# Performance work log

Measured on AMD Instinct MI355X. Metric: run time of the kernel, lower is better.

The kernel has to match this reference:

```python
import jax, jax.numpy as jnp
import numpy as np

D = 512      # feature_bins
DK = 64      # d_k = d_v
H = 8        # n_heads
EPS = 1e-5


def setup_inputs() -> dict:
    key = jax.random.key(0)
    ks = jax.random.split(key, 12)
    B, S = 4, 2048
    s = 1.0 / np.sqrt(D)
    inp = {
        "Q": jax.random.normal(ks[0], (B, S, D), jnp.float32),
        "K": jax.random.normal(ks[1], (B, S, D), jnp.float32),
        "V": jax.random.normal(ks[2], (B, S, D), jnp.float32),
        # nn.Linear params: weight [out, in], bias [out]
        "Wq": jax.random.normal(ks[3], (H * DK, D), jnp.float32) * s,
        "bq": jnp.zeros((H * DK,), jnp.float32),
        "Wk": jax.random.normal(ks[4], (H * DK, D), jnp.float32) * s,
        "bk": jnp.zeros((H * DK,), jnp.float32),
        "Wv": jax.random.normal(ks[5], (H * DK, D), jnp.float32) * s,
        "bv": jnp.zeros((H * DK,), jnp.float32),
        "Wo": jax.random.normal(ks[6], (D, H * DK), jnp.float32) * s,
        "bo": jnp.zeros((D,), jnp.float32),
        "gamma": jnp.ones((D,), jnp.float32),
        "beta": jnp.zeros((D,), jnp.float32),
    }
    return inp


def _layernorm(x, gamma, beta):
    mu = jnp.mean(x, axis=-1, keepdims=True)
    var = jnp.mean(jnp.square(x - mu), axis=-1, keepdims=True)
    return (x - mu) * jax.lax.rsqrt(var + EPS) * gamma + beta


def reference(Q, K, V, Wq, bq, Wk, bk, Wv, bv, Wo, bo, gamma, beta):
    B, S, _ = Q.shape
    residual = Q
    # projections -> [B, H, S, DK]
    q = (Q @ Wq.T + bq).reshape(B, S, H, DK).transpose(0, 2, 1, 3)
    k = (K @ Wk.T + bk).reshape(B, S, H, DK).transpose(0, 2, 1, 3)
    v = (V @ Wv.T + bv).reshape(B, S, H, DK).transpose(0, 2, 1, 3)
    # NOTE: original code has NO 1/sqrt(d_k) scaling
    scores = jnp.einsum("bhqd,bhkd->bhqk", q, k)
    attn = jax.nn.softmax(scores, axis=-1)
    context = jnp.einsum("bhqk,bhkd->bhqd", attn, v)
    context = context.transpose(0, 2, 1, 3).reshape(B, S, H * DK)
    output = context @ Wo.T + bo
    out = _layernorm(output + residual, gamma, beta)
    return (out, attn)
```

## Files before the change

### kernel.cpp

```cpp
#include <hip/hip_runtime.h>

#define NB 4
#define NS 2048
#define ND 512
#define NH 8
#define NDK 64
#define LN_EPS 1e-5f
#define SCLAMP 80.0f

typedef __attribute__((ext_vector_type(8))) short short8;
typedef __attribute__((ext_vector_type(4))) short s16x4;
typedef __attribute__((ext_vector_type(4))) float f32x4;

__device__ inline short f2bf(float x) {
    unsigned u = __builtin_bit_cast(unsigned, x);
    unsigned r = (u + 0x7FFFu + ((u >> 16) & 1u)) >> 16;
    return (short)r;
}
__device__ inline float bf2f(short h) {
    unsigned u = ((unsigned)(unsigned short)h) << 16;
    return __builtin_bit_cast(float, u);
}
__device__ inline unsigned splitT(float x) {
    unsigned u = __builtin_bit_cast(unsigned, x);
    unsigned h = u >> 16;
    float r = x - bf2f((short)h);
    unsigned l = __builtin_bit_cast(unsigned, r) >> 16;
    return (h & 0xFFFFu) | (l << 16);
}

__device__ inline int swzS(int row, int b8) {
    return row * 64 + (((b8) * 8) ^ ((row & 7) << 3));
}
__device__ inline int swz4(int row, int g4) {
    return row * 64 + ((((g4 >> 1)) * 8) ^ ((row & 7) << 3)) + (g4 & 1) * 4;
}

template<int MODE>
__global__ __launch_bounds__(256) void k_projm(
    const float* __restrict__ X, const float* __restrict__ W,
    const float* __restrict__ bias,
    short* __restrict__ outh, short* __restrict__ outl)
{
    __shared__ short WsH[8192], WsL[8192];
    const int tid = threadIdx.x;
    const int w = tid >> 6, lane = tid & 63;
    const int lr = lane & 15, lg = lane >> 4;
    const int row0 = blockIdx.y * 64;
    const int col0 = blockIdx.x * 128;
    const int xrow = row0 + w * 16 + lr;

    f32x4 acc[8] = {};

    float4 wb[8], ab[4];
#pragma unroll
    for (int i = 0; i < 8; ++i) {
        int idx = tid + 256 * i, wrow = idx >> 4, g4 = idx & 15;
        wb[i] = *(const float4*)&W[(size_t)(col0 + wrow) * ND + g4 * 4];
    }
#pragma unroll
    for (int ks = 0; ks < 2; ++ks) {
        ab[2*ks+0] = *(const float4*)&X[(size_t)xrow * ND + ks * 32 + lg * 8];
        ab[2*ks+1] = *(const float4*)&X[(size_t)xrow * ND + ks * 32 + lg * 8 + 4];
    }

    for (int kc = 0; kc < 8; ++kc) {
        __syncthreads();
#pragma unroll
        for (int i = 0; i < 8; ++i) {
            int idx = tid + 256 * i, wrow = idx >> 4, g4 = idx & 15;
            s16x4 hv, lv;
            unsigned p0 = splitT(wb[i].x), p1 = splitT(wb[i].y);
            unsigned p2 = splitT(wb[i].z), p3 = splitT(wb[i].w);
            hv[0] = (short)p0; lv[0] = (short)(p0 >> 16);
            hv[1] = (short)p1; lv[1] = (short)(p1 >> 16);
            hv[2] = (short)p2; lv[2] = (short)(p2 >> 16);
            hv[3] = (short)p3; lv[3] = (short)(p3 >> 16);
            int off = swz4(wrow, g4);
            *(s16x4*)&WsH[off] = hv;
            *(s16x4*)&WsL[off] = lv;
        }
        __syncthreads();

        short8 ah[2], al[2];
#pragma unroll
        for (int ks = 0; ks < 2; ++ks) {
#pragma unroll
            for (int j = 0; j < 4; ++j) {
                unsigned p = splitT(ab[2*ks][j]);
                ah[ks][j] = (short)p; al[ks][j] = (short)(p >> 16);
            }
#pragma unroll
            for (int j = 0; j < 4; ++j) {
                unsigned p = splitT(ab[2*ks+1][j]);
                ah[ks][4+j] = (short)p; al[ks][4+j] = (short)(p >> 16);
            }
        }

        if (kc < 7) {
            const int kn = (kc + 1) * 64;
#pragma unroll
            for (int i = 0; i < 8; ++i) {
                int idx = tid + 256 * i, wrow = idx >> 4, g4 = idx & 15;
                wb[i] = *(const float4*)&W[(size_t)(col0 + wrow) * ND + kn + g4 * 4];
            }
#pragma unroll
            for (int ks = 0; ks < 2; ++ks) {
                ab[2*ks+0] = *(const float4*)&X[(size_t)xrow * ND + kn + ks * 32 + lg * 8];
                ab[2*ks+1] = *(const float4*)&X[(size_t)xrow * ND + kn + ks * 32 + lg * 8 + 4];
            }
        }

#pragma unroll
        for (int cs = 0; cs < 8; ++cs)
#pragma unroll
            for (int ks = 0; ks < 2; ++ks) {
                short8 fh = *(const short8*)&WsH[swzS(cs * 16 + lr, ks * 4 + lg)];
                short8 fl = *(const short8*)&WsL[swzS(cs * 16 + lr, ks * 4 + lg)];
                acc[cs] = __builtin_amdgcn_mfma_f32_16x16x32_bf16(ah[ks], fh, acc[cs], 0, 0, 0);
                acc[cs] = __builtin_amdgcn_mfma_f32_16x16x32_bf16(ah[ks], fl, acc[cs], 0, 0, 0);
                acc[cs] = __builtin_amdgcn_mfma_f32_16x16x32_bf16(al[ks], fh, acc[cs], 0, 0, 0);
            }
    }

#pragma unroll
    for (int cs = 0; cs < 8; ++cs) {
        int c = col0 + cs * 16 + lr;
        int h_ = c >> 6, dk = c & (NDK - 1);
        float bv = bias[c];
#pragma unroll
        for (int r = 0; r < 4; ++r) {
            int gr = row0 + w * 16 + lg * 4 + r;
            int b_ = gr >> 11, s_ = gr & (NS - 1);
            float x = acc[cs][r] + bv;
            if (MODE == 0) {
                size_t idx = (((size_t)b_ * NH + h_) * NS + s_) * NDK + dk;
                short hb = f2bf(x);
                outh[idx] = hb;
                outl[idx] = f2bf(x - bf2f(hb));
            } else {
                size_t idx = (((size_t)b_ * NH + h_) * NDK + dk) * NS + s_;
                outh[idx] = f2bf(x);
            }
        }
    }
}

__device__ inline void att_decode(int wg, int& bh, int& rt) {
    rt = (wg >> 3) & 31;
    bh = (wg & 7) + ((wg >> 8) << 3);
}

__global__ __launch_bounds__(256) void k_pvl(
    const short* __restrict__ qh, const short* __restrict__ ql,
    const short* __restrict__ kh, const short* __restrict__ kl,
    const short* __restrict__ vtb,
    float* __restrict__ iLrow, short* __restrict__ ctxb)
{
    __shared__ short KsH[4096], KsL[4096], Vs[4096];
    __shared__ short plbf[4][16][72];
    const int tid = threadIdx.x;
    const int w = tid >> 6, lane = tid & 63;
    const int lr = lane & 15, lg = lane >> 4;
    int bh, rt;
    att_decode(blockIdx.x, bh, rt);
    const int row0 = rt * 64 + w * 16;
    const size_t base = (size_t)bh * NS * NDK;
    const short* vb = vtb + (size_t)bh * NDK * NS;
    const int srow0 = tid >> 3, sb8 = tid & 7;
    const int srow1 = srow0 + 32;

    short8 ah[2], al[2];
#pragma unroll
    for (int ks = 0; ks < 2; ++ks) {
        size_t idx = base + (size_t)(row0 + lr) * NDK + ks * 32 + lg * 8;
        ah[ks] = *(const short8*)&qh[idx];
        al[ks] = *(const short8*)&ql[idx];
    }

    float lsum[4] = {0.f, 0.f, 0.f, 0.f};
    f32x4 vacc[4] = {};

    short8 nh0, nh1, nl0, nl1, nv0, nv1;
    {
        nh0 = *(const short8*)&kh[base + (size_t)(srow0) * NDK + sb8 * 8];
        nh1 = *(const short8*)&kh[base + (size_t)(srow1) * NDK + sb8 * 8];
        nl0 = *(const short8*)&kl[base + (size_t)(srow0) * NDK + sb8 * 8];
        nl1 = *(const short8*)&kl[base + (size_t)(srow1) * NDK + sb8 * 8];
        nv0 = *(const short8*)&vb[(size_t)srow0 * NS + sb8 * 8];
        nv1 = *(const short8*)&vb[(size_t)srow1 * NS + sb8 * 8];
    }

    for (int c = 0; c < 32; ++c) {
        short8 ch0 = nh0, ch1 = nh1, cl0 = nl0, cl1 = nl1, cv0 = nv0, cv1 = nv1;
        __syncthreads();
        *(short8*)&KsH[swzS(srow0, sb8)] = ch0;
        *(short8*)&KsH[swzS(srow1, sb8)] = ch1;
        *(short8*)&KsL[swzS(srow0, sb8)] = cl0;
        *(short8*)&KsL[swzS(srow1, sb8)] = cl1;
        *(short8*)&Vs[swzS(srow0, sb8)] = cv0;
        *(short8*)&Vs[swzS(srow1, sb8)] = cv1;
        __syncthreads();

        if (c < 31) {
            const int coln = (c + 1) * 64;
            nh0 = *(const short8*)&kh[base + (size_t)(coln + srow0) * NDK + sb8 * 8];
            nh1 = *(const short8*)&kh[base + (size_t)(coln + srow1) * NDK + sb8 * 8];
            nl0 = *(const short8*)&kl[base + (size_t)(coln + srow0) * NDK + sb8 * 8];
            nl1 = *(const short8*)&kl[base + (size_t)(coln + srow1) * NDK + sb8 * 8];
            nv0 = *(const short8*)&vb[(size_t)srow0 * NS + coln + sb8 * 8];
            nv1 = *(const short8*)&vb[(size_t)srow1 * NS + coln + sb8 * 8];
        }

        f32x4 sa[4] = {};
#pragma unroll
        for (int cs = 0; cs < 4; ++cs)
#pragma unroll
            for (int ks = 0; ks < 2; ++ks) {
                short8 fh = *(const short8*)&KsH[swzS(cs * 16 + lr, ks * 4 + lg)];
                short8 fl = *(const short8*)&KsL[swzS(cs * 16 + lr, ks * 4 + lg)];
                sa[cs] = __builtin_amdgcn_mfma_f32_16x16x32_bf16(ah[ks], fh, sa[cs], 0, 0, 0);
                sa[cs] = __builtin_amdgcn_mfma_f32_16x16x32_bf16(ah[ks], fl, sa[cs], 0, 0, 0);
                sa[cs] = __builtin_amdgcn_mfma_f32_16x16x32_bf16(al[ks], fh, sa[cs], 0, 0, 0);
            }

#pragma unroll
        for (int cs = 0; cs < 4; ++cs)
#pragma unroll
            for (int r = 0; r < 4; ++r) {
                float e = __expf(fminf(sa[cs][r], SCLAMP));
                lsum[r] += e;
                plbf[w][lg * 4 + r][cs * 16 + lr] = f2bf(e);
            }
#pragma unroll
        for (int k2 = 0; k2 < 2; ++k2) {
            short8 pa = *(const short8*)&plbf[w][lr][k2 * 32 + lg * 8];
#pragma unroll
            for (int d = 0; d < 4; ++d) {
                short8 vf = *(const short8*)&Vs[swzS(d * 16 + lr, k2 * 4 + lg)];
                vacc[d] = __builtin_amdgcn_mfma_f32_16x16x32_bf16(pa, vf, vacc[d], 0, 0, 0);
            }
        }
    }

#pragma unroll
    for (int r = 0; r < 4; ++r)
#pragma unroll
        for (int off = 1; off < 16; off <<= 1)
            lsum[r] += __shfl_xor(lsum[r], off);

    float iL[4];
#pragma unroll
    for (int r = 0; r < 4; ++r) iL[r] = 1.0f / lsum[r];
    if (lr == 0) {
#pragma unroll
        for (int r = 0; r < 4; ++r)
            iLrow[(size_t)bh * NS + row0 + lg * 4 + r] = iL[r];
    }
    const int b_ = bh >> 3, h_ = bh & 7;
#pragma unroll
    for (int d = 0; d < 4; ++d)
#pragma unroll
        for (int r = 0; r < 4; ++r) {
            int row = row0 + lg * 4 + r;
            ctxb[((size_t)b_ * NS + row) * ND + h_ * NDK + d * 16 + lr] =
                f2bf(vacc[d][r] * iL[r]);
        }
}

__global__ __launch_bounds__(256) void k_attn_write(
    const short* __restrict__ qh, const short* __restrict__ ql,
    const short* __restrict__ kh, const short* __restrict__ kl,
    const float* __restrict__ iLrow, float* __restrict__ attn)
{
    __shared__ short KsH[4096], KsL[4096];
    const int tid = threadIdx.x;
    const int w = tid >> 6, lane = tid & 63;
    const int lr = lane & 15, lg = lane >> 4;
    int bh, rt;
    att_decode(blockIdx.x, bh, rt);
    const int row0 = rt * 64 + w * 16;
    const size_t base = (size_t)bh * NS * NDK;
    float* ab = attn + (size_t)bh * NS * NS;
    const int srow0 = tid >> 3, sb8 = tid & 7;
    const int srow1 = srow0 + 32;

    short8 ah[2], al[2];
#pragma unroll
    for (int ks = 0; ks < 2; ++ks) {
        size_t idx = base + (size_t)(row0 + lr) * NDK + ks * 32 + lg * 8;
        ah[ks] = *(const short8*)&qh[idx];
        al[ks] = *(const short8*)&ql[idx];
    }
    float iLr[4];
#pragma unroll
    for (int r = 0; r < 4; ++r)
        iLr[r] = iLrow[(size_t)bh * NS + row0 + lg * 4 + r];

    short8 nh0, nh1, nl0, nl1;
    {
        nh0 = *(const short8*)&kh[base + (size_t)(srow0) * NDK + sb8 * 8];
        nh1 = *(const short8*)&kh[base + (size_t)(srow1) * NDK + sb8 * 8];
        nl0 = *(const short8*)&kl[base + (size_t)(srow0) * NDK + sb8 * 8];
        nl1 = *(const short8*)&kl[base + (size_t)(srow1) * NDK + sb8 * 8];
    }

    for (int c = 0; c < 32; ++c) {
        short8 ch0 = nh0, ch1 = nh1, cl0 = nl0, cl1 = nl1;
        __syncthreads();
        *(short8*)&KsH[swzS(srow0, sb8)] = ch0;
        *(short8*)&KsH[swzS(srow1, sb8)] = ch1;
        *(short8*)&KsL[swzS(srow0, sb8)] = cl0;
        *(short8*)&KsL[swzS(srow1, sb8)] = cl1;
        __syncthreads();

        if (c < 31) {
            const int coln = (c + 1) * 64;
            nh0 = *(const short8*)&kh[base + (size_t)(coln + srow0) * NDK + sb8 * 8];
            nh1 = *(const short8*)&kh[base + (size_t)(coln + srow1) * NDK + sb8 * 8];
            nl0 = *(const short8*)&kl[base + (size_t)(coln + srow0) * NDK + sb8 * 8];
            nl1 = *(const short8*)&kl[base + (size_t)(coln + srow1) * NDK + sb8 * 8];
        }

        const int col0 = c * 64;
        f32x4 sa[4] = {};
#pragma unroll
        for (int cs = 0; cs < 4; ++cs)
#pragma unroll
            for (int ks = 0; ks < 2; ++ks) {
                short8 fh = *(const short8*)&KsH[swzS(cs * 16 + lr, ks * 4 + lg)];
                short8 fl = *(const short8*)&KsL[swzS(cs * 16 + lr, ks * 4 + lg)];
                sa[cs] = __builtin_amdgcn_mfma_f32_16x16x32_bf16(ah[ks], fh, sa[cs], 0, 0, 0);
                sa[cs] = __builtin_amdgcn_mfma_f32_16x16x32_bf16(ah[ks], fl, sa[cs], 0, 0, 0);
                sa[cs] = __builtin_amdgcn_mfma_f32_16x16x32_bf16(al[ks], fh, sa[cs], 0, 0, 0);
            }

#pragma unroll
        for (int cs = 0; cs < 4; ++cs)
#pragma unroll
            for (int r = 0; r < 4; ++r) {
                float p = __expf(fminf(sa[cs][r], SCLAMP)) * iLr[r];
                ab[(size_t)(row0 + lg * 4 + r) * NS + col0 + cs * 16 + lr] = p;
            }
    }
}

__global__ __launch_bounds__(256) void k_outproj_m(
    const short* __restrict__ Xc, const float* __restrict__ W,
    const float* __restrict__ bias, const float* __restrict__ Qin,
    float* __restrict__ out)
{
    __shared__ short WsH[8192], WsL[8192];
    const int tid = threadIdx.x;
    const int w = tid >> 6, lane = tid & 63;
    const int lr = lane & 15, lg = lane >> 4;
    const int row0 = blockIdx.y * 64;
    const int col0 = blockIdx.x * 128;
    const int xrow = row0 + w * 16 + lr;

    f32x4 acc[8] = {};

    float4 wb[8];
    short8 abn[2];
#pragma unroll
    for (int i = 0; i < 8; ++i) {
        int idx = tid + 256 * i, wrow = idx >> 4, g4 = idx & 15;
        wb[i] = *(const float4*)&W[(size_t)(col0 + wrow) * ND + g4 * 4];
    }
#pragma unroll
    for (int ks = 0; ks < 2; ++ks)
        abn[ks] = *(const short8*)&Xc[(size_t)xrow * ND + ks * 32 + lg * 8];

    for (int kc = 0; kc < 8; ++kc) {
        __syncthreads();
#pragma unroll
        for (int i = 0; i < 8; ++i) {
            int idx = tid + 256 * i, wrow = idx >> 4, g4 = idx & 15;
            s16x4 hv, lv;
            unsigned p0 = splitT(wb[i].x), p1 = splitT(wb[i].y);
            unsigned p2 = splitT(wb[i].z), p3 = splitT(wb[i].w);
            hv[0] = (short)p0; lv[0] = (short)(p0 >> 16);
            hv[1] = (short)p1; lv[1] = (short)(p1 >> 16);
            hv[2] = (short)p2; lv[2] = (short)(p2 >> 16);
            hv[3] = (short)p3; lv[3] = (short)(p3 >> 16);
            int off = swz4(wrow, g4);
            *(s16x4*)&WsH[off] = hv;
            *(s16x4*)&WsL[off] = lv;
        }
        __syncthreads();

        short8 ah[2] = { abn[0], abn[1] };

        if (kc < 7) {
            const int kn = (kc + 1) * 64;
#pragma unroll
            for (int i = 0; i < 8; ++i) {
                int idx = tid + 256 * i, wrow = idx >> 4, g4 = idx & 15;
                wb[i] = *(const float4*)&W[(size_t)(col0 + wrow) * ND + kn + g4 * 4];
            }
#pragma unroll
            for (int ks = 0; ks < 2; ++ks)
                abn[ks] = *(const short8*)&Xc[(size_t)xrow * ND + kn + ks * 32 + lg * 8];
        }

#pragma unroll
        for (int cs = 0; cs < 8; ++cs)
#pragma unroll
            for (int ks = 0; ks < 2; ++ks) {
                short8 fh = *(const short8*)&WsH[swzS(cs * 16 + lr, ks * 4 + lg)];
                short8 fl = *(const short8*)&WsL[swzS(cs * 16 + lr, ks * 4 + lg)];
                acc[cs] = __builtin_amdgcn_mfma_f32_16x16x32_bf16(ah[ks], fh, acc[cs], 0, 0, 0);
                acc[cs] = __builtin_amdgcn_mfma_f32_16x16x32_bf16(ah[ks], fl, acc[cs], 0, 0, 0);
            }
    }

#pragma unroll
    for (int cs = 0; cs < 8; ++cs) {
        int c = col0 + cs * 16 + lr;
        float bv = bias[c];
#pragma unroll
        for (int r = 0; r < 4; ++r) {
            int gr = row0 + w * 16 + lg * 4 + r;
            float res = Qin[(size_t)gr * ND + c];
            out[(size_t)gr * ND + c] = acc[cs][r] + bv + res;
        }
    }
}

__global__ __launch_bounds__(256) void k_ln(
    float* __restrict__ out, const float* __restrict__ gamma,
    const float* __restrict__ beta)
{
    const int tid = threadIdx.x;
    float* p = out + (size_t)blockIdx.x * ND;
    float2 v = *(const float2*)&p[tid * 2];

    float s = v.x + v.y;
#pragma unroll
    for (int off = 32; off > 0; off >>= 1) s += __shfl_xor(s, off);
    __shared__ float red1[4];
    __shared__ float red2[4];
    if ((tid & 63) == 0) red1[tid >> 6] = s;
    __syncthreads();
    const float mu = (red1[0] + red1[1] + red1[2] + red1[3]) * (1.0f / ND);

    float dx = v.x - mu, dy = v.y - mu;
    float q = dx * dx + dy * dy;
#pragma unroll
    for (int off = 32; off > 0; off >>= 1) q += __shfl_xor(q, off);
    if ((tid & 63) == 0) red2[tid >> 6] = q;
    __syncthreads();
    const float var = (red2[0] + red2[1] + red2[2] + red2[3]) * (1.0f / ND);
    const float inv = rsqrtf(var + LN_EPS);

    float2 g = *(const float2*)&gamma[tid * 2];
    float2 be = *(const float2*)&beta[tid * 2];
    float2 o = { dx * inv * g.x + be.x, dy * inv * g.y + be.y };
    *(float2*)&p[tid * 2] = o;
}

extern "C" void kernel_launch(void* const* d_in, const int* in_sizes, int n_in,
                              void* d_out, int out_size, void* d_ws, size_t ws_size,
                              hipStream_t stream)
{
    const float* Q    = (const float*)d_in[0];
    const float* K    = (const float*)d_in[1];
    const float* V    = (const float*)d_in[2];
    const float* Wq   = (const float*)d_in[3];
    const float* bq   = (const float*)d_in[4];
    const float* Wk   = (const float*)d_in[5];
    const float* bk   = (const float*)d_in[6];
    const float* Wv   = (const float*)d_in[7];
    const float* bv   = (const float*)d_in[8];
    const float* Wo   = (const float*)d_in[9];
    const float* bo   = (const float*)d_in[10];
    const float* gam  = (const float*)d_in[11];
    const float* bet  = (const float*)d_in[12];

    float* out  = (float*)d_out;
    float* attn = out + (size_t)NB * NS * ND;

    const size_t QKV = (size_t)NB * NH * NS * NDK;
    short* qh   = (short*)d_ws;
    short* ql   = qh + QKV;
    short* kh   = ql + QKV;
    short* kl   = kh + QKV;
    short* vtb  = kl + QKV;
    short* ctxb = vtb + QKV;
    float* iLrow = (float*)(ctxb + QKV);

    dim3 blk(256);

    dim3 gP(ND / 128, (NB * NS) / 64);
    k_projm<0><<<gP, blk, 0, stream>>>(Q, Wq, bq, qh, ql);
    k_projm<0><<<gP, blk, 0, stream>>>(K, Wk, bk, kh, kl);
    k_projm<1><<<gP, blk, 0, stream>>>(V, Wv, bv, vtb, (short*)nullptr);

    dim3 gAtt((NS / 64) * NB * NH);
    k_pvl<<<gAtt, blk, 0, stream>>>(qh, ql, kh, kl, vtb, iLrow, ctxb);
    k_attn_write<<<gAtt, blk, 0, stream>>>(qh, ql, kh, kl, iLrow, attn);

    dim3 gO(ND / 128, (NB * NS) / 64);
    k_outproj_m<<<gO, blk, 0, stream>>>(ctxb, Wo, bo, Q, out);

    k_ln<<<dim3(NB * NS), blk, 0, stream>>>(out, gam, bet);
}
```

Before: 352.2 us.

## Process two 64-row query subtiles per workgroup in attention kernels

Each workgroup in both attention kernels now covers 128 query rows instead of 64. Every wave handles two 16-row subtiles, so the K and V tiles staged in shared memory are reused twice and the grid shrinks by half. This is meant to cut global and LDS traffic for K/V staging per query row. The cost is more registers for Q fragments and accumulators, plus only 512 workgroups, which may lower occupancy or leave part of the 256 CUs idle.

```diff
diff --git a/kernel.cpp b/kernel.cpp
--- a/kernel.cpp
+++ b/kernel.cpp
@@ -146,9 +146,9 @@
     }
 }
 
-__device__ inline void att_decode(int wg, int& bh, int& rt) {
-    rt = (wg >> 3) & 31;
-    bh = (wg & 7) + ((wg >> 8) << 3);
+__device__ inline void att_decode2(int wg, int& bh, int& rt) {
+    rt = (wg >> 3) & 15;
+    bh = (wg & 7) + ((wg >> 7) << 3);
 }
 
 __global__ __launch_bounds__(256) void k_pvl(
@@ -158,28 +158,30 @@
     float* __restrict__ iLrow, short* __restrict__ ctxb)
 {
     __shared__ short KsH[4096], KsL[4096], Vs[4096];
-    __shared__ short plbf[4][16][72];
+    __shared__ short plbf[4][32][72];
     const int tid = threadIdx.x;
     const int w = tid >> 6, lane = tid & 63;
     const int lr = lane & 15, lg = lane >> 4;
     int bh, rt;
-    att_decode(blockIdx.x, bh, rt);
-    const int row0 = rt * 64 + w * 16;
+    att_decode2(blockIdx.x, bh, rt);
+    const int row0 = rt * 128 + w * 16;
     const size_t base = (size_t)bh * NS * NDK;
     const short* vb = vtb + (size_t)bh * NDK * NS;
     const int srow0 = tid >> 3, sb8 = tid & 7;
     const int srow1 = srow0 + 32;
 
-    short8 ah[2], al[2];
-#pragma unroll
-    for (int ks = 0; ks < 2; ++ks) {
-        size_t idx = base + (size_t)(row0 + lr) * NDK + ks * 32 + lg * 8;
-        ah[ks] = *(const short8*)&qh[idx];
-        al[ks] = *(const short8*)&ql[idx];
-    }
-
-    float lsum[4] = {0.f, 0.f, 0.f, 0.f};
-    f32x4 vacc[4] = {};
+    short8 ah[2][2], al[2][2];
+#pragma unroll
+    for (int st = 0; st < 2; ++st)
+#pragma unroll
+        for (int ks = 0; ks < 2; ++ks) {
+            size_t idx = base + (size_t)(row0 + st * 64 + lr) * NDK + ks * 32 + lg * 8;
+            ah[st][ks] = *(const short8*)&qh[idx];
+            al[st][ks] = *(const short8*)&ql[idx];
+        }
+
+    float lsum[2][4] = {};
+    f32x4 vacc[2][4] = {};
 
     short8 nh0, nh1, nl0, nl1, nv0, nv1;
     {
@@ -212,60 +214,76 @@
             nv1 = *(const short8*)&vb[(size_t)srow1 * NS + coln + sb8 * 8];
         }
 
-        f32x4 sa[4] = {};
+        f32x4 sa[2][4] = {};
 #pragma unroll
         for (int cs = 0; cs < 4; ++cs)
 #pragma unroll
             for (int ks = 0; ks < 2; ++ks) {
                 short8 fh = *(const short8*)&KsH[swzS(cs * 16 + lr, ks * 4 + lg)];
                 short8 fl = *(const short8*)&KsL[swzS(cs * 16 + lr, ks * 4 + lg)];
-                sa[cs] = __builtin_amdgcn_mfma_f32_16x16x32_bf16(ah[ks], fh, sa[cs], 0, 0, 0);
-                sa[cs] = __builtin_amdgcn_mfma_f32_16x16x32_bf16(ah[ks], fl, sa[cs], 0, 0, 0);
-                sa[cs] = __builtin_amdgcn_mfma_f32_16x16x32_bf16(al[ks], fh, sa[cs], 0, 0, 0);
-            }
-
-#pragma unroll
-        for (int cs = 0; cs < 4; ++cs)
-#pragma unroll
-            for (int r = 0; r < 4; ++r) {
-                float e = __expf(fminf(sa[cs][r], SCLAMP));
-                lsum[r] += e;
-                plbf[w][lg * 4 + r][cs * 16 + lr] = f2bf(e);
-            }
+#pragma unroll
+                for (int st = 0; st < 2; ++st) {
+                    sa[st][cs] = __builtin_amdgcn_mfma_f32_16x16x32_bf16(ah[st][ks], fh, sa[st][cs], 0, 0, 0);
+                    sa[st][cs] = __builtin_amdgcn_mfma_f32_16x16x32_bf16(ah[st][ks], fl, sa[st][cs], 0, 0, 0);
+                    sa[st][cs] = __builtin_amdgcn_mfma_f32_16x16x32_bf16(al[st][ks], fh, sa[st][cs], 0, 0, 0);
+                }
+            }
+
+#pragma unroll
+        for (int st = 0; st < 2; ++st)
+#pragma unroll
+            for (int cs = 0; cs < 4; ++cs)
+#pragma unroll
+                for (int r = 0; r < 4; ++r) {
+                    float e = __expf(fminf(sa[st][cs][r], SCLAMP));
+                    lsum[st][r] += e;
+                    plbf[w][st * 16 + lg * 4 + r][cs * 16 + lr] = f2bf(e);
+                }
+
 #pragma unroll
         for (int k2 = 0; k2 < 2; ++k2) {
-            short8 pa = *(const short8*)&plbf[w][lr][k2 * 32 + lg * 8];
+            short8 pa0 = *(const short8*)&plbf[w][lr][k2 * 32 + lg * 8];
+            short8 pa1 = *(const short8*)&plbf[w][16 + lr][k2 * 32 + lg * 8];
 #pragma unroll
             for (int d = 0; d < 4; ++d) {
                 short8 vf = *(const short8*)&Vs[swzS(d * 16 + lr, k2 * 4 + lg)];
-                vacc[d] = __builtin_amdgcn_mfma_f32_16x16x32_bf16(pa, vf, vacc[d], 0, 0, 0);
-            }
-        }
-    }
-
-#pragma unroll
-    for (int r = 0; r < 4; ++r)
-#pragma unroll
-        for (int off = 1; off < 16; off <<= 1)
-            lsum[r] += __shfl_xor(lsum[r], off);
-
-    float iL[4];
-#pragma unroll
-    for (int r = 0; r < 4; ++r) iL[r] = 1.0f / lsum[r];
+                vacc[0][d] = __builtin_amdgcn_mfma_f32_16x16x32_bf16(pa0, vf, vacc[0][d], 0, 0, 0);
+                vacc[1][d] = __builtin_amdgcn_mfma_f32_16x16x32_bf16(pa1, vf, vacc[1][d], 0, 0, 0);
+            }
+        }
+    }
+
+#pragma unroll
+    for (int st = 0; st < 2; ++st)
+#pragma unroll
+        for (int r = 0; r < 4; ++r)
+#pragma unroll
+            for (int off = 1; off < 16; off <<= 1)
+                lsum[st][r] += __shfl_xor(lsum[st][r], off);
+
+    float iL[2][4];
+#pragma unroll
+    for (int st = 0; st < 2; ++st)
+#pragma unroll
+        for (int r = 0; r < 4; ++r) iL[st][r] = 1.0f / lsum[st][r];
     if (lr == 0) {
 #pragma unroll
-        for (int r = 0; r < 4; ++r)
-            iLrow[(size_t)bh * NS + row0 + lg * 4 + r] = iL[r];
+        for (int st = 0; st < 2; ++st)
+#pragma unroll
+            for (int r = 0; r < 4; ++r)
+                iLrow[(size_t)bh * NS + row0 + st * 64 + lg * 4 + r] = iL[st][r];
     }
     const int b_ = bh >> 3, h_ = bh & 7;
 #pragma unroll
-    for (int d = 0; d < 4; ++d)
-#pragma unroll
-        for (int r = 0; r < 4; ++r) {
-            int row = row0 + lg * 4 + r;
-            ctxb[((size_t)b_ * NS + row) * ND + h_ * NDK + d * 16 + lr] =
-                f2bf(vacc[d][r] * iL[r]);
-        }
+    for (int st = 0; st < 2; ++st)
+#pragma unroll
+        for (int d = 0; d < 4; ++d)
+#pragma unroll
+            for (int r = 0; r < 4; ++r) {
+                int row = row0 + st * 64 + lg * 4 + r;
+                ctxb[((size_t)b_ * NS + row) * ND + h_ * NDK + d * 16 + lr] =
+                    f2bf(vacc[st][d][r] * iL[st][r]);
+            }
 }
 
 __global__ __launch_bounds__(256) void k_attn_write(
@@ -278,24 +296,28 @@
     const int w = tid >> 6, lane = tid & 63;
     const int lr = lane & 15, lg = lane >> 4;
     int bh, rt;
-    att_decode(blockIdx.x, bh, rt);
-    const int row0 = rt * 64 + w * 16;
+    att_decode2(blockIdx.x, bh, rt);
+    const int row0 = rt * 128 + w * 16;
     const size_t base = (size_t)bh * NS * NDK;
     float* ab = attn + (size_t)bh * NS * NS;
     const int srow0 = tid >> 3, sb8 = tid & 7;
     const int srow1 = srow0 + 32;
 
-    short8 ah[2], al[2];
-#pragma unroll
-    for (int ks = 0; ks < 2; ++ks) {
-        size_t idx = base + (size_t)(row0 + lr) * NDK + ks * 32 + lg * 8;
-        ah[ks] = *(const short8*)&qh[idx];
-        al[ks] = *(const short8*)&ql[idx];
-    }
-    float iLr[4];
-#pragma unroll
-    for (int r = 0; r < 4; ++r)
-        iLr[r] = iLrow[(size_t)bh * NS + row0 + lg * 4 + r];
+    short8 ah[2][2], al[2][2];
+#pragma unroll
+    for (int st = 0; st < 2; ++st)
+#pragma unroll
+        for (int ks = 0; ks < 2; ++ks) {
+            size_t idx = base + (size_t)(row0 + st * 64 + lr) * NDK + ks * 32 + lg * 8;
+            ah[st][ks] = *(const short8*)&qh[idx];
+            al[st][ks] = *(const short8*)&ql[idx];
+        }
+    float iLr[2][4];
+#pragma unroll
+    for (int st = 0; st < 2; ++st)
+#pragma unroll
+        for (int r = 0; r < 4; ++r)
+            iLr[st][r] = iLrow[(size_t)bh * NS + row0 + st * 64 + lg * 4 + r];
 
     short8 nh0, nh1, nl0, nl1;
     {
@@ -323,25 +345,30 @@
         }
 
         const int col0 = c * 64;
-        f32x4 sa[4] = {};
+        f32x4 sa[2][4] = {};
 #pragma unroll
         for (int cs = 0; cs < 4; ++cs)
 #pragma unroll
             for (int ks = 0; ks < 2; ++ks) {
                 short8 fh = *(const short8*)&KsH[swzS(cs * 16 + lr, ks * 4 + lg)];
                 short8 fl = *(const short8*)&KsL[swzS(cs * 16 + lr, ks * 4 + lg)];
-                sa[cs] = __builtin_amdgcn_mfma_f32_16x16x32_bf16(ah[ks], fh, sa[cs], 0, 0, 0);
-                sa[cs] = __builtin_amdgcn_mfma_f32_16x16x32_bf16(ah[ks], fl, sa[cs], 0, 0, 0);
-                sa[cs] = __builtin_amdgcn_mfma_f32_16x16x32_bf16(al[ks], fh, sa[cs], 0, 0, 0);
-            }
-
-#pragma unroll
-        for (int cs = 0; cs < 4; ++cs)
-#pragma unroll
-            for (int r = 0; r < 4; ++r) {
-                float p = __expf(fminf(sa[cs][r], SCLAMP)) * iLr[r];
-                ab[(size_t)(row0 + lg * 4 + r) * NS + col0 + cs * 16 + lr] = p;
-            }
+#pragma unroll
+                for (int st = 0; st < 2; ++st) {
+                    sa[st][cs] = __builtin_amdgcn_mfma_f32_16x16x32_bf16(ah[st][ks], fh, sa[st][cs], 0, 0, 0);
+                    sa[st][cs] = __builtin_amdgcn_mfma_f32_16x16x32_bf16(ah[st][ks], fl, sa[st][cs], 0, 0, 0);
+                    sa[st][cs] = __builtin_amdgcn_mfma_f32_16x16x32_bf16(al[st][ks], fh, sa[st][cs], 0, 0, 0);
+                }
+            }
+
+#pragma unroll
+        for (int st = 0; st < 2; ++st)
+#pragma unroll
+            for (int cs = 0; cs < 4; ++cs)
+#pragma unroll
+                for (int r = 0; r < 4; ++r) {
+                    float p = __expf(fminf(sa[st][cs][r], SCLAMP)) * iLr[st][r];
+                    ab[(size_t)(row0 + st * 64 + lg * 4 + r) * NS + col0 + cs * 16 + lr] = p;
+                }
     }
 }
 
@@ -496,7 +523,7 @@
     k_projm<0><<<gP, blk, 0, stream>>>(K, Wk, bk, kh, kl);
     k_projm<1><<<gP, blk, 0, stream>>>(V, Wv, bv, vtb, (short*)nullptr);
 
-    dim3 gAtt((NS / 64) * NB * NH);
+    dim3 gAtt((NS / 128) * NB * NH);
     k_pvl<<<gAtt, blk, 0, stream>>>(qh, ql, kh, kl, vtb, iLrow, ctxb);
     k_attn_write<<<gAtt, blk, 0, stream>>>(qh, ql, kh, kl, iLrow, attn);
 
```

New measurement: 332.0 us. 5.7% less time.
